# Kernel optimization log

Hardware: AMD Instinct MI355X
Metric: run time of the kernel (lower is better)

Reference implementation:

```python
import jax, jax.numpy as jnp
import numpy as np

K = 5            # kernel_size per pseudo-dim
N = 51200        # nodes
E = 819200       # edges (avg degree 16)
B = 64           # graphs in batch

# 2^dim corner offsets for degree-1 (linear) open B-spline in dim=2
_BITS = jnp.array([[0, 0], [0, 1], [1, 0], [1, 1]], dtype=jnp.int32)  # [4,2]

def spline_basis(pseudo):
    # pseudo: [E,2] in [0,1]. Returns basis [E,4], weight indices [E,4].
    v = pseudo * (K - 1)
    lo = jnp.clip(jnp.floor(v).astype(jnp.int32), 0, K - 2)   # [E,2]
    frac = v - lo.astype(pseudo.dtype)                        # [E,2]
    idx = lo[:, None, :] + _BITS[None]                        # [E,4,2]
    w = jnp.where(_BITS[None] == 1, frac[:, None, :], 1.0 - frac[:, None, :])
    basis = w.prod(-1)                                        # [E,4]
    widx = idx[..., 0] * K + idx[..., 1]                      # [E,4] in [0,25)
    return basis, widx

def spline_conv(x, src, dst, basis, widx, W, root, bias):
    # x:[N,Fin], W:[25,Fin,Fout], root:[Fin,Fout], bias:[Fout]
    n = x.shape[0]
    Z = jnp.einsum('ni,kio->nko', x, W)          # [N,25,Fout] per-node per-kernel transforms
    Zg = Z[src[:, None], widx]                   # [E,4,Fout] irregular gather
    msg = jnp.einsum('es,eso->eo', basis, Zg)    # [E,Fout]
    agg = jax.ops.segment_sum(msg, dst, num_segments=n)
    deg = jax.ops.segment_sum(jnp.ones_like(msg[:, 0]), dst, num_segments=n)
    agg = agg / jnp.maximum(deg, 1.0)[:, None]   # mean aggregation
    return agg + x @ root + bias

def setup_inputs():
    key = jax.random.key(0)
    ks = jax.random.split(key, 12)
    x = jax.random.normal(ks[0], (N, 7), jnp.float32)
    edge_index = jax.random.randint(ks[1], (2, E), 0, N, dtype=jnp.int32)
    pseudo = jax.random.uniform(ks[2], (E, 2), jnp.float32)
    slices = jnp.arange(B + 1, dtype=jnp.int32) * (N // B)   # graph boundaries
    W1 = jax.random.normal(ks[3], (K * K, 7, 32), jnp.float32) * 0.2
    root1 = jax.random.normal(ks[4], (7, 32), jnp.float32) * 0.2
    b1 = jnp.zeros((32,), jnp.float32)
    W2 = jax.random.normal(ks[5], (K * K, 32, 64), jnp.float32) * 0.1
    root2 = jax.random.normal(ks[6], (32, 64), jnp.float32) * 0.1
    b2 = jnp.zeros((64,), jnp.float32)
    fc_w = jax.random.normal(ks[7], (64, 30), jnp.float32) * 0.1
    fc_b = jnp.zeros((30,), jnp.float32)
    return {"x": x, "edge_index": edge_index, "pseudo": pseudo, "slices": slices,
            "W1": W1, "root1": root1, "b1": b1, "W2": W2, "root2": root2,
            "b2": b2, "fc_w": fc_w, "fc_b": fc_b}

def reference(x, edge_index, pseudo, slices, W1, root1, b1, W2, root2, b2, fc_w, fc_b):
    src, dst = edge_index[0], edge_index[1]
    basis, widx = spline_basis(pseudo)
    h = jax.nn.elu(spline_conv(x, src, dst, basis, widx, W1, root1, b1))
    h = jax.nn.elu(spline_conv(h, src, dst, basis, widx, W2, root2, b2))
    # batch_average: mean of node features per graph (slices = boundaries)
    gid = jnp.clip(jnp.searchsorted(slices, jnp.arange(N), side='right') - 1, 0, B - 1)
    sums = jax.ops.segment_sum(h, gid, num_segments=B)
    counts = (slices[1:] - slices[:-1]).astype(h.dtype)
    g = sums / jnp.maximum(counts, 1.0)[:, None]             # [B,64]
    # dropout is identity in eval mode
    logits = g @ fc_w + fc_b
    return jax.nn.log_softmax(logits, axis=-1)
```

## Files before the change

### kernel.cpp

```cpp
#include <hip/hip_runtime.h>
#include <hip/hip_fp16.h>
#include <math.h>

#define N_NODES 51200
#define N_EDGES 819200
#define NB 64
#define CAP 64

typedef _Float16 half8 __attribute__((ext_vector_type(8)));
typedef __attribute__((ext_vector_type(4))) float float4v;

__device__ __forceinline__ float eluf(float x) {
  return x > 0.f ? x : expm1f(x);
}

__device__ __forceinline__ void dec2(int w0, int w1, int c, float& basf, int& Kc) {
  int K = w0 >> 16;
  float f0 = __half2float(__ushort_as_half((unsigned short)(w1 & 0xFFFF)));
  float f1 = __half2float(__ushort_as_half((unsigned short)(((unsigned)w1) >> 16)));
  float b0 = (c & 2) ? f0 : 1.f - f0;
  float bv = (c & 1) ? f1 : 1.f - f1;
  Kc = K + (c >> 1) * 5 + (c & 1);
  basf = b0 * bv;
}

__device__ __forceinline__ void rmw16(unsigned* Tr, int Kc, int q, float bf, int4 hv) {
  __half2 bas = __float2half2_rn(bf);
  __half2* tp = (__half2*)&Tr[Kc * 16 + q * 4];
  const __half2* h = (const __half2*)&hv;
  __half2 t0 = tp[0], t1 = tp[1], t2 = tp[2], t3 = tp[3];
  tp[0] = __hfma2(bas, h[0], t0);
  tp[1] = __hfma2(bas, h[1], t1);
  tp[2] = __hfma2(bas, h[2], t2);
  tp[3] = __hfma2(bas, h[3], t3);
}

__global__ __launch_bounds__(256) void prep(const float* __restrict__ x,
                                            const float* __restrict__ W1,
                                            const float* __restrict__ root1,
                                            const float* __restrict__ W2,
                                            const float* __restrict__ root2,
                                            __half* __restrict__ xh,
                                            __half* __restrict__ W1T,
                                            __half* __restrict__ W2T,
                                            float* __restrict__ gbuf) {
  int b = blockIdx.x, tid = threadIdx.x;
  if (b < 1600) {
    int idx = b * 256 + tid;
    int n = idx >> 3, j = idx & 7;
    xh[idx] = __float2half((j < 7) ? x[n * 7 + j] : 0.f);
  } else if (b < 1628) {
    int idx = (b - 1600) * 256 + tid;
    int o = idx / 224, k = idx - o * 224;
    float v = 0.f;
    if (k < 200) {
      int cell = k >> 3, f = k & 7;
      if (f < 7) v = W1[(cell * 7 + f) * 32 + o];
    } else if (k < 207) {
      v = root1[(k - 200) * 32 + o];
    }
    W1T[idx] = __float2half(v);
  } else if (b < 1836) {
    int idx = (b - 1628) * 256 + tid;
    int o = idx / 832, k = idx - o * 832;
    float v = (k < 800) ? W2[k * 64 + o] : root2[(k - 800) * 64 + o];
    W2T[idx] = __float2half(v);
  } else {
    int idx = (b - 1836) * 256 + tid;
    gbuf[idx] = 0.f;
  }
}

__global__ __launch_bounds__(256) void scatter_eid(const int* __restrict__ ei,
                                                   const float* __restrict__ pseudo,
                                                   int* __restrict__ cnt,
                                                   int2* __restrict__ bucket) {
  int base = blockIdx.x * 2048 + threadIdx.x;
#pragma unroll
  for (int u = 0; u < 8; u++) {
    int e = base + u * 256;
    int src = ei[e], dst = ei[N_EDGES + e];
    float v0 = pseudo[2 * e] * 4.f;
    float v1 = pseudo[2 * e + 1] * 4.f;
    int lo0 = min(max((int)floorf(v0), 0), 3);
    int lo1 = min(max((int)floorf(v1), 0), 3);
    float f0 = v0 - (float)lo0, f1 = v1 - (float)lo1;
    int K = lo0 * 5 + lo1;
    unsigned short u0 = __half_as_ushort(__float2half(f0));
    unsigned short u1 = __half_as_ushort(__float2half(f1));
    int w0 = src | (K << 16);
    int w1 = (int)((unsigned)u0 | ((unsigned)u1 << 16));
    int slot = atomicAdd(&cnt[dst], 1);
    if (slot < CAP) bucket[(size_t)dst * CAP + slot] = make_int2(w0, w1);
  }
}

__global__ __launch_bounds__(256) void build_perm(const int* __restrict__ cnt,
                                                  int* __restrict__ perm) {
  __shared__ int hist[65];
  __shared__ int base_s[65];
  int g = blockIdx.x, tid = threadIdx.x;
  int n0 = g * 800;
  if (tid < 65) hist[tid] = 0;
  __syncthreads();
  for (int i = tid; i < 800; i += 256) {
    int d = min(cnt[n0 + i], 64);
    atomicAdd(&hist[d], 1);
  }
  __syncthreads();
  if (tid == 0) {
    int s = 0;
    for (int b = 0; b < 65; b++) { base_s[b] = s; s += hist[b]; }
  }
  __syncthreads();
  for (int i = tid; i < 800; i += 256) {
    int d = min(cnt[n0 + i], 64);
    int pos = atomicAdd(&base_s[d], 1);
    perm[n0 + pos] = n0 + i;
  }
}

#define L1N 16
__global__ __launch_bounds__(256) void fused_l1(const int2* __restrict__ bucket,
                                                const int* __restrict__ cnt,
                                                const int* __restrict__ perm,
                                                const unsigned* __restrict__ xh,
                                                const __half* __restrict__ W1T,
                                                const float* __restrict__ b1,
                                                unsigned short* __restrict__ h1h) {
  __shared__ unsigned T[L1N * 112];
  __shared__ float invdeg_s[L1N];
  __shared__ int pn_s[L1N];
  int tid = threadIdx.x;
  int n0 = blockIdx.x * L1N;
  for (int idx = tid; idx < L1N * 112; idx += 256) T[idx] = 0u;
  if (tid < L1N) {
    int pn = perm[n0 + tid];
    pn_s[tid] = pn;
    invdeg_s[tid] = 1.f / fmaxf((float)cnt[pn], 1.f);
  }
  __syncthreads();
  if (tid < L1N * 4) {
    int row = tid >> 2, p = tid & 3;
    int n = pn_s[row];
    float dgc = fmaxf((float)cnt[n], 1.f);
    unsigned xv = xh[n * 4 + p];
    __half2 h = __hmul2(*(const __half2*)&xv, __float2half2_rn(dgc));
    T[row * 112 + 100 + p] = *(unsigned*)&h;
  }
  int wv = tid >> 6, l = tid & 63;
  int slot = l >> 4, c = (l >> 2) & 3, p = l & 3;
  int nn = wv * 4 + slot;
  int n = pn_s[nn];
  int dg = min(cnt[n], CAP);
  int dmax = dg;
  dmax = max(dmax, __shfl_xor(dmax, 16));
  dmax = max(dmax, __shfl_xor(dmax, 32));
  const int2* bk = bucket + (size_t)n * CAP;
  unsigned* Tr = &T[nn * 112];
  int4 ra0 = *(const int4*)(bk + 0);
  int4 rb0 = *(const int4*)(bk + 2);
  int4 ra1 = *(const int4*)(bk + 4);
  int4 rb1 = *(const int4*)(bk + 6);
  unsigned xv0 = xh[(ra0.x & 0xFFFF) * 4 + p];
  unsigned xv1 = xh[(ra0.z & 0xFFFF) * 4 + p];
  unsigned xv2 = xh[(rb0.x & 0xFFFF) * 4 + p];
  unsigned xv3 = xh[(rb0.z & 0xFFFF) * 4 + p];
  for (int j = 0; j < dmax; j += 4) {
    int jp = min(j + 8, CAP - 4);
    int4 ra2 = *(const int4*)(bk + jp);
    int4 rb2 = *(const int4*)(bk + jp + 2);
    unsigned nx0 = xh[(ra1.x & 0xFFFF) * 4 + p];
    unsigned nx1 = xh[(ra1.z & 0xFFFF) * 4 + p];
    unsigned nx2 = xh[(rb1.x & 0xFFFF) * 4 + p];
    unsigned nx3 = xh[(rb1.z & 0xFFFF) * 4 + p];
    bool a0 = j < dg, a1 = j + 1 < dg, a2 = j + 2 < dg, a3 = j + 3 < dg;
    float bf; int Kc;
    if (a0) { dec2(ra0.x, ra0.y, c, bf, Kc);
      __half2* tp = (__half2*)&Tr[Kc * 4 + p];
      *tp = __hfma2(__float2half2_rn(bf), *(const __half2*)&xv0, *tp); }
    if (a1) { dec2(ra0.z, ra0.w, c, bf, Kc);
      __half2* tp = (__half2*)&Tr[Kc * 4 + p];
      *tp = __hfma2(__float2half2_rn(bf), *(const __half2*)&xv1, *tp); }
    if (a2) { dec2(rb0.x, rb0.y, c, bf, Kc);
      __half2* tp = (__half2*)&Tr[Kc * 4 + p];
      *tp = __hfma2(__float2half2_rn(bf), *(const __half2*)&xv2, *tp); }
    if (a3) { dec2(rb0.z, rb0.w, c, bf, Kc);
      __half2* tp = (__half2*)&Tr[Kc * 4 + p];
      *tp = __hfma2(__float2half2_rn(bf), *(const __half2*)&xv3, *tp); }
    ra0 = ra1; rb0 = rb1; ra1 = ra2; rb1 = rb2;
    xv0 = nx0; xv1 = nx1; xv2 = nx2; xv3 = nx3;
  }
  __syncthreads();
  if (wv < 2) {
    int m = l & 15, quad = l >> 4;
    const char* abase = (const char*)T + m * 448 + quad * 16;
    const __half* bbase = W1T + (wv * 16 + m) * 224 + quad * 8;
    float4v acc = {0.f, 0.f, 0.f, 0.f};
#pragma unroll
    for (int it = 0; it < 7; it++) {
      half8 af = *(const half8*)(abase + it * 64);
      half8 bf = *(const half8*)(bbase + it * 32);
      acc = __builtin_amdgcn_mfma_f32_16x16x32_f16(af, bf, acc, 0, 0, 0);
    }
    int feat = wv * 16 + m;
    float bb = b1[feat];
#pragma unroll
    for (int r = 0; r < 4; r++) {
      int row = quad * 4 + r;
      float v = eluf(acc[r] * invdeg_s[row] + bb);
      h1h[(size_t)pn_s[row] * 32 + feat] = __half_as_ushort(__float2half(v));
    }
  }
}

#define L2N 16
__global__ __launch_bounds__(256) void fused_l2(const int2* __restrict__ bucket,
                                                const int* __restrict__ cnt,
                                                const int* __restrict__ perm,
                                                const unsigned* __restrict__ h1hu,
                                                const __half* __restrict__ W2T,
                                                const float* __restrict__ b2,
                                                float* __restrict__ gbuf) {
  __shared__ unsigned T16[L2N * 420];
  __shared__ float invdeg_s[L2N];
  __shared__ int pn_s[L2N];
  int tid = threadIdx.x;
  int n0 = blockIdx.x * L2N;
  for (int idx = tid; idx < L2N * 420; idx += 256) T16[idx] = 0u;
  if (tid < L2N) {
    int pn = perm[n0 + tid];
    pn_s[tid] = pn;
    invdeg_s[tid] = 1.f / fmaxf((float)cnt[pn], 1.f);
  }
  __syncthreads();
  {
    int row = tid >> 4, p = tid & 15;
    int n = pn_s[row];
    float dgc = fmaxf((float)cnt[n], 1.f);
    unsigned hv = h1hu[(size_t)n * 16 + p];
    __half2 h = __hmul2(*(const __half2*)&hv, __float2half2_rn(dgc));
    T16[row * 420 + 400 + p] = *(unsigned*)&h;
  }
  int wv = tid >> 6, l = tid & 63;
  int slot = l >> 4, c = (l >> 2) & 3, q = l & 3;
  int nn = wv * 4 + slot;
  int n = pn_s[nn];
  int dg = min(cnt[n], CAP);
  int dmax = dg;
  dmax = max(dmax, __shfl_xor(dmax, 16));
  dmax = max(dmax, __shfl_xor(dmax, 32));
  const int2* bk = bucket + (size_t)n * CAP;
  unsigned* Tr = &T16[nn * 420];
  const unsigned* h1q = h1hu + q * 4;
  int4 ra0 = *(const int4*)(bk + 0);
  int4 rb0 = *(const int4*)(bk + 2);
  int4 ra1 = *(const int4*)(bk + 4);
  int4 rb1 = *(const int4*)(bk + 6);
  int4 hv0 = *(const int4*)(h1q + (size_t)(ra0.x & 0xFFFF) * 16);
  int4 hv1 = *(const int4*)(h1q + (size_t)(ra0.z & 0xFFFF) * 16);
  int4 hv2 = *(const int4*)(h1q + (size_t)(rb0.x & 0xFFFF) * 16);
  int4 hv3 = *(const int4*)(h1q + (size_t)(rb0.z & 0xFFFF) * 16);
  for (int j = 0; j < dmax; j += 4) {
    int jp = min(j + 8, CAP - 4);
    int4 ra2 = *(const int4*)(bk + jp);
    int4 rb2 = *(const int4*)(bk + jp + 2);
    int4 nh0 = *(const int4*)(h1q + (size_t)(ra1.x & 0xFFFF) * 16);
    int4 nh1 = *(const int4*)(h1q + (size_t)(ra1.z & 0xFFFF) * 16);
    int4 nh2 = *(const int4*)(h1q + (size_t)(rb1.x & 0xFFFF) * 16);
    int4 nh3 = *(const int4*)(h1q + (size_t)(rb1.z & 0xFFFF) * 16);
    bool a0 = j < dg, a1 = j + 1 < dg, a2 = j + 2 < dg, a3 = j + 3 < dg;
    float bf; int Kc;
    if (a0) { dec2(ra0.x, ra0.y, c, bf, Kc); rmw16(Tr, Kc, q, bf, hv0); }
    if (a1) { dec2(ra0.z, ra0.w, c, bf, Kc); rmw16(Tr, Kc, q, bf, hv1); }
    if (a2) { dec2(rb0.x, rb0.y, c, bf, Kc); rmw16(Tr, Kc, q, bf, hv2); }
    if (a3) { dec2(rb0.z, rb0.w, c, bf, Kc); rmw16(Tr, Kc, q, bf, hv3); }
    ra0 = ra1; rb0 = rb1; ra1 = ra2; rb1 = rb2;
    hv0 = nh0; hv1 = nh1; hv2 = nh2; hv3 = nh3;
  }
  __syncthreads();
  int m = l & 15, quad = l >> 4;
  const char* abase = (const char*)T16 + m * 1680 + quad * 16;
  const __half* bbase = W2T + (size_t)(wv * 16 + m) * 832 + quad * 8;
  float4v acc = {0.f, 0.f, 0.f, 0.f};
  for (int it = 0; it < 26; it++) {
    half8 af = *(const half8*)(abase + it * 64);
    half8 bf = *(const half8*)(bbase + it * 32);
    acc = __builtin_amdgcn_mfma_f32_16x16x32_f16(af, bf, acc, 0, 0, 0);
  }
  int feat = wv * 16 + m;
  float bb = b2[feat];
  float psum = 0.f;
#pragma unroll
  for (int r = 0; r < 4; r++) {
    int node = quad * 4 + r;
    psum += eluf(acc[r] * invdeg_s[node] + bb);
  }
  psum += __shfl_xor(psum, 16);
  psum += __shfl_xor(psum, 32);
  if (l < 16) {
    int g = n0 / 800;
    atomicAdd(&gbuf[g * 64 + feat], psum);
  }
}

__global__ __launch_bounds__(64) void fc_ls(const float* __restrict__ gbuf,
                                            const int* __restrict__ slices,
                                            const float* __restrict__ fcw,
                                            const float* __restrict__ fcb,
                                            float* __restrict__ out) {
  int g = blockIdx.x;
  int l = threadIdx.x;
  float scale = 1.f / fmaxf((float)(slices[g + 1] - slices[g]), 1.f);
  float logit = -INFINITY;
  if (l < 30) {
    float acc = fcb[l];
    for (int i = 0; i < 64; i++) acc += gbuf[g * 64 + i] * scale * fcw[i * 30 + l];
    logit = acc;
  }
  float m = logit;
  for (int off = 16; off; off >>= 1) m = fmaxf(m, __shfl_xor(m, off, 32));
  float e = (l < 30) ? expf(logit - m) : 0.f;
  for (int off = 16; off; off >>= 1) e += __shfl_xor(e, off, 32);
  if (l < 30) out[g * 30 + l] = logit - m - logf(e);
}

extern "C" void kernel_launch(void* const* d_in, const int* in_sizes, int n_in,
                              void* d_out, int out_size, void* d_ws, size_t ws_size,
                              hipStream_t stream) {
  const float* x      = (const float*)d_in[0];
  const int*   ei     = (const int*)d_in[1];
  const float* pseudo = (const float*)d_in[2];
  const int*   slices = (const int*)d_in[3];
  const float* W1     = (const float*)d_in[4];
  const float* root1  = (const float*)d_in[5];
  const float* b1     = (const float*)d_in[6];
  const float* W2     = (const float*)d_in[7];
  const float* root2  = (const float*)d_in[8];
  const float* b2     = (const float*)d_in[9];
  const float* fcw    = (const float*)d_in[10];
  const float* fcb    = (const float*)d_in[11];
  float* out = (float*)d_out;

  char* ws = (char*)d_ws;
  int*      cnt    = (int*)ws;
  int2*     bucket = (int2*)(cnt + N_NODES);
  unsigned* h1h    = (unsigned*)(bucket + (size_t)N_NODES * CAP);
  float*    gbuf   = (float*)(h1h + (size_t)N_NODES * 16);
  unsigned* xh     = (unsigned*)(gbuf + 64 * 64);
  __half*   W1T    = (__half*)(xh + (size_t)N_NODES * 4);
  __half*   W2T    = W1T + 32 * 224;
  int*      perm   = (int*)(W2T + 64 * 832);

  hipMemsetAsync(cnt, 0, N_NODES * sizeof(int), stream);

  prep<<<1852, 256, 0, stream>>>(x, W1, root1, W2, root2,
                                 (__half*)xh, W1T, W2T, gbuf);
  scatter_eid<<<N_EDGES / 2048, 256, 0, stream>>>(ei, pseudo, cnt, bucket);
  build_perm<<<NB, 256, 0, stream>>>(cnt, perm);
  fused_l1<<<N_NODES / L1N, 256, 0, stream>>>(bucket, cnt, perm, xh, W1T, b1,
                                              (unsigned short*)h1h);
  fused_l2<<<N_NODES / L2N, 256, 0, stream>>>(bucket, cnt, perm, h1h, W2T, b2,
                                              gbuf);
  fc_ls<<<NB, 64, 0, stream>>>(gbuf, slices, fcw, fcb, out);
}
```

Baseline: 211.1 us.

## Merge prep and edge scatter kernels, vectorize LDS zeroing, prefetch MFMA B operand

Folds the edge-scatter kernel into the prep kernel as extra blocks, removing one kernel launch and letting the two independent workloads run concurrently. The shared-memory zeroing loops in both fused layers now use 16-byte stores instead of 4-byte ones. The layer-2 MFMA loop software-prefetches the next weight fragment from global memory to hide load latency. The merged kernel mixes a heavy atomic workload with light conversion blocks, which may change how blocks are scheduled.

```diff
diff --git a/kernel.cpp b/kernel.cpp
--- a/kernel.cpp
+++ b/kernel.cpp
@@ -35,22 +35,43 @@
   tp[3] = __hfma2(bas, h[3], t3);
 }
 
-__global__ __launch_bounds__(256) void prep(const float* __restrict__ x,
-                                            const float* __restrict__ W1,
-                                            const float* __restrict__ root1,
-                                            const float* __restrict__ W2,
-                                            const float* __restrict__ root2,
-                                            __half* __restrict__ xh,
-                                            __half* __restrict__ W1T,
-                                            __half* __restrict__ W2T,
-                                            float* __restrict__ gbuf) {
+__global__ __launch_bounds__(256) void prep_scatter(
+    const float* __restrict__ x, const float* __restrict__ W1,
+    const float* __restrict__ root1, const float* __restrict__ W2,
+    const float* __restrict__ root2, __half* __restrict__ xh,
+    __half* __restrict__ W1T, __half* __restrict__ W2T,
+    float* __restrict__ gbuf, const int* __restrict__ ei,
+    const float* __restrict__ pseudo, int* __restrict__ cnt,
+    int2* __restrict__ bucket) {
   int b = blockIdx.x, tid = threadIdx.x;
-  if (b < 1600) {
-    int idx = b * 256 + tid;
+  if (b < 400) {
+    int base = b * 2048 + tid;
+#pragma unroll
+    for (int u = 0; u < 8; u++) {
+      int e = base + u * 256;
+      int src = ei[e], dst = ei[N_EDGES + e];
+      float v0 = pseudo[2 * e] * 4.f;
+      float v1 = pseudo[2 * e + 1] * 4.f;
+      int lo0 = min(max((int)floorf(v0), 0), 3);
+      int lo1 = min(max((int)floorf(v1), 0), 3);
+      float f0 = v0 - (float)lo0, f1 = v1 - (float)lo1;
+      int K = lo0 * 5 + lo1;
+      unsigned short u0 = __half_as_ushort(__float2half(f0));
+      unsigned short u1 = __half_as_ushort(__float2half(f1));
+      int w0 = src | (K << 16);
+      int w1 = (int)((unsigned)u0 | ((unsigned)u1 << 16));
+      int slot = atomicAdd(&cnt[dst], 1);
+      if (slot < CAP) bucket[(size_t)dst * CAP + slot] = make_int2(w0, w1);
+    }
+    return;
+  }
+  int bb = b - 400;
+  if (bb < 1600) {
+    int idx = bb * 256 + tid;
     int n = idx >> 3, j = idx & 7;
     xh[idx] = __float2half((j < 7) ? x[n * 7 + j] : 0.f);
-  } else if (b < 1628) {
-    int idx = (b - 1600) * 256 + tid;
+  } else if (bb < 1628) {
+    int idx = (bb - 1600) * 256 + tid;
     int o = idx / 224, k = idx - o * 224;
     float v = 0.f;
     if (k < 200) {
@@ -60,38 +81,14 @@
       v = root1[(k - 200) * 32 + o];
     }
     W1T[idx] = __float2half(v);
-  } else if (b < 1836) {
-    int idx = (b - 1628) * 256 + tid;
+  } else if (bb < 1836) {
+    int idx = (bb - 1628) * 256 + tid;
     int o = idx / 832, k = idx - o * 832;
     float v = (k < 800) ? W2[k * 64 + o] : root2[(k - 800) * 64 + o];
     W2T[idx] = __float2half(v);
   } else {
-    int idx = (b - 1836) * 256 + tid;
+    int idx = (bb - 1836) * 256 + tid;
     gbuf[idx] = 0.f;
-  }
-}
-
-__global__ __launch_bounds__(256) void scatter_eid(const int* __restrict__ ei,
-                                                   const float* __restrict__ pseudo,
-                                                   int* __restrict__ cnt,
-                                                   int2* __restrict__ bucket) {
-  int base = blockIdx.x * 2048 + threadIdx.x;
-#pragma unroll
-  for (int u = 0; u < 8; u++) {
-    int e = base + u * 256;
-    int src = ei[e], dst = ei[N_EDGES + e];
-    float v0 = pseudo[2 * e] * 4.f;
-    float v1 = pseudo[2 * e + 1] * 4.f;
-    int lo0 = min(max((int)floorf(v0), 0), 3);
-    int lo1 = min(max((int)floorf(v1), 0), 3);
-    float f0 = v0 - (float)lo0, f1 = v1 - (float)lo1;
-    int K = lo0 * 5 + lo1;
-    unsigned short u0 = __half_as_ushort(__float2half(f0));
-    unsigned short u1 = __half_as_ushort(__float2half(f1));
-    int w0 = src | (K << 16);
-    int w1 = (int)((unsigned)u0 | ((unsigned)u1 << 16));
-    int slot = atomicAdd(&cnt[dst], 1);
-    if (slot < CAP) bucket[(size_t)dst * CAP + slot] = make_int2(w0, w1);
   }
 }
 
@@ -133,7 +130,8 @@
   __shared__ int pn_s[L1N];
   int tid = threadIdx.x;
   int n0 = blockIdx.x * L1N;
-  for (int idx = tid; idx < L1N * 112; idx += 256) T[idx] = 0u;
+  for (int idx = tid; idx < 448; idx += 256)
+    ((int4*)T)[idx] = make_int4(0, 0, 0, 0);
   if (tid < L1N) {
     int pn = perm[n0 + tid];
     pn_s[tid] = pn;
@@ -227,7 +225,8 @@
   __shared__ int pn_s[L2N];
   int tid = threadIdx.x;
   int n0 = blockIdx.x * L2N;
-  for (int idx = tid; idx < L2N * 420; idx += 256) T16[idx] = 0u;
+  for (int idx = tid; idx < 1680; idx += 256)
+    ((int4*)T16)[idx] = make_int4(0, 0, 0, 0);
   if (tid < L2N) {
     int pn = perm[n0 + tid];
     pn_s[tid] = pn;
@@ -283,10 +282,12 @@
   const char* abase = (const char*)T16 + m * 1680 + quad * 16;
   const __half* bbase = W2T + (size_t)(wv * 16 + m) * 832 + quad * 8;
   float4v acc = {0.f, 0.f, 0.f, 0.f};
+  half8 bf0 = *(const half8*)(bbase);
   for (int it = 0; it < 26; it++) {
+    half8 bfn = *(const half8*)(bbase + min(it + 1, 25) * 32);
     half8 af = *(const half8*)(abase + it * 64);
-    half8 bf = *(const half8*)(bbase + it * 32);
-    acc = __builtin_amdgcn_mfma_f32_16x16x32_f16(af, bf, acc, 0, 0, 0);
+    acc = __builtin_amdgcn_mfma_f32_16x16x32_f16(af, bf0, acc, 0, 0, 0);
+    bf0 = bfn;
   }
   int feat = wv * 16 + m;
   float bb = b2[feat];
@@ -354,9 +355,9 @@
 
   hipMemsetAsync(cnt, 0, N_NODES * sizeof(int), stream);
 
-  prep<<<1852, 256, 0, stream>>>(x, W1, root1, W2, root2,
-                                 (__half*)xh, W1T, W2T, gbuf);
-  scatter_eid<<<N_EDGES / 2048, 256, 0, stream>>>(ei, pseudo, cnt, bucket);
+  prep_scatter<<<2252, 256, 0, stream>>>(x, W1, root1, W2, root2,
+                                         (__half*)xh, W1T, W2T, gbuf,
+                                         ei, pseudo, cnt, bucket);
   build_perm<<<NB, 256, 0, stream>>>(cnt, perm);
   fused_l1<<<N_NODES / L1N, 256, 0, stream>>>(bucket, cnt, perm, xh, W1T, b1,
                                               (unsigned short*)h1h);
```

New measurement: 211.5 us, median of 5. No clear change (+0.2%).
